# Kernel tuning notes

Measured on AMD Instinct MI355X. Metric: run time of the kernel, lower is better.

The kernel has to match this reference:

```python
import jax, jax.numpy as jnp
import numpy as np

DIM = 256
N_EMBED = 8192


def setup_inputs() -> dict:
    key = jax.random.key(0)
    k1, k2 = jax.random.split(key)
    x = jax.random.normal(k1, (16, 32, 32, DIM), dtype=jnp.float32)
    embed = jax.random.normal(k2, (DIM, N_EMBED), dtype=jnp.float32)
    return {"x": x, "embed": embed}


def reference(x, embed):
    # x: [B, H, W, D]; embed: [D, K]
    D = embed.shape[0]
    flat = x.reshape(-1, D)  # [N, D]
    dist = (
        jnp.sum(flat * flat, axis=1, keepdims=True)
        - 2.0 * (flat @ embed)
        + jnp.sum(embed * embed, axis=0, keepdims=True)
    )  # [N, K]
    embed_ind = jnp.argmin(dist, axis=1)  # argmax of -dist
    embed_ind = embed_ind.reshape(x.shape[:-1])  # [B, H, W]
    quantize = jnp.take(embed.T, embed_ind, axis=0)  # [B, H, W, D]
    diff = jnp.mean((jax.lax.stop_gradient(quantize) - x) ** 2)
    quantize = x + jax.lax.stop_gradient(quantize - x)  # straight-through
    return quantize, diff, embed_ind
```

## Files before the change

kernel.cpp:

```cpp
#include <hip/hip_runtime.h>

typedef unsigned long long u64;
typedef unsigned short ushort_t;
typedef float f32x4 __attribute__((ext_vector_type(4)));
typedef short bf16x8 __attribute__((ext_vector_type(8)));
typedef unsigned short ushort8 __attribute__((ext_vector_type(8)));

#define D_DIM   256
#define N_ROWS  16384
#define K_CODES 8192
#define OFF_DIFF 4194304
#define OFF_IND  4194305

#define XH_OFF    0ULL
#define XL_OFF    8388608ULL
#define EHT_OFF   16777216ULL
#define ELT_OFF   20971520ULL
#define ETF_OFF   25165824ULL
#define ENORM_OFF 33554432ULL
#define KEYS_OFF  33587200ULL
#define PV1_OFF   33718272ULL
#define PIDX_OFF  37912576ULL
#define PV2_OFF   42106880ULL
#define WLC_OFF   46301184ULL
#define WL_OFF    46301440ULL
#define PART_OFF  46366976ULL
#define WS_NEED   46375168ULL

#define MARGIN_TH 0.08f

#define GLD(gp, lp) __builtin_amdgcn_global_load_lds( \
    (const __attribute__((address_space(1))) unsigned int*)(const void*)(gp), \
    (__attribute__((address_space(3))) unsigned int*)(void*)(lp), 16, 0, 0)

__device__ __forceinline__ unsigned int fsort(float f) {
    unsigned int u = __float_as_uint(f);
    return (u & 0x80000000u) ? ~u : (u | 0x80000000u);
}
__device__ __forceinline__ ushort_t f2bf(float f) {
    unsigned int u = __float_as_uint(f);
    unsigned int r = (u + 0x7fffu + ((u >> 16) & 1u)) >> 16;
    return (ushort_t)r;
}
__device__ __forceinline__ float bf2f(ushort_t h) {
    return __uint_as_float(((unsigned int)h) << 16);
}

__global__ __launch_bounds__(256) void k_prep(const float* __restrict__ x,
                                              const float* __restrict__ e,
                                              ushort_t* __restrict__ xh,
                                              ushort_t* __restrict__ xl,
                                              ushort_t* __restrict__ ehT,
                                              ushort_t* __restrict__ elT,
                                              float* __restrict__ enorm,
                                              int* __restrict__ wlc,
                                              float* __restrict__ out_diff) {
    __shared__ float tile[64][257];
    const int bid = blockIdx.x;
    const int t = threadIdx.x;
    if (bid < 2048) {
        int base = (bid * 256 + t) * 8;
        float4 v0 = *reinterpret_cast<const float4*>(&x[base]);
        float4 v1 = *reinterpret_cast<const float4*>(&x[base + 4]);
        float f[8] = {v0.x, v0.y, v0.z, v0.w, v1.x, v1.y, v1.z, v1.w};
        ushort8 h, l;
        #pragma unroll
        for (int i = 0; i < 8; ++i) {
            ushort_t hb = f2bf(f[i]);
            h[i] = hb;
            l[i] = f2bf(f[i] - bf2f(hb));
        }
        *reinterpret_cast<ushort8*>(&xh[base]) = h;
        *reinterpret_cast<ushort8*>(&xl[base]) = l;
    } else if (bid < 2176) {
        const int c0 = (bid - 2048) * 64;
        for (int it = 0; it < 64; ++it) {
            int d = it * 4 + (t >> 6);
            tile[t & 63][d] = e[d * K_CODES + c0 + (t & 63)];
        }
        __syncthreads();
        #pragma unroll
        for (int it = 0; it < 8; ++it) {
            int cc = it * 8 + (t >> 5);
            int d0 = (t & 31) * 8;
            ushort8 h8, l8;
            #pragma unroll
            for (int j = 0; j < 8; ++j) {
                float v = tile[cc][d0 + j];
                ushort_t hb = f2bf(v);
                h8[j] = hb;
                l8[j] = f2bf(v - bf2f(hb));
            }
            size_t o = (size_t)(c0 + cc) * 256 + d0;
            *reinterpret_cast<ushort8*>(&ehT[o]) = h8;
            *reinterpret_cast<ushort8*>(&elT[o]) = l8;
        }
    } else {
        int k = (bid - 2176) * 256 + t;
        float s = 0.f;
        #pragma unroll 8
        for (int d = 0; d < D_DIM; ++d) {
            float v = e[d * K_CODES + k];
            s = fmaf(v, v, s);
        }
        enorm[k] = s;
        if (k == 0) { *wlc = 0; out_diff[0] = 0.0f; }
    }
}

__global__ __launch_bounds__(256, 3) void k_mfma(const ushort_t* __restrict__ xh,
                                                 const ushort_t* __restrict__ xl,
                                                 const ushort_t* __restrict__ ehT,
                                                 const ushort_t* __restrict__ elT,
                                                 const float* __restrict__ enorm,
                                                 float* __restrict__ pv1,
                                                 int* __restrict__ pidx,
                                                 float* __restrict__ pv2) {
    __shared__ short Ah[4096], Al[4096], Bh[4096], Bl[4096];
    __shared__ float mg_v1[2][128];
    __shared__ float mg_v2[2][128];
    __shared__ int   mg_i1[2][128];
    const int tid = threadIdx.x;
    const int l = tid & 63, w = tid >> 6;
    const int wm = w >> 1, wn = w & 1;
    const int r0 = blockIdx.x * 128;
    const int c0 = blockIdx.y * 128;

    const int rl = l >> 2;
    const int g = (l & 3) ^ ((rl >> 1) & 3);
    const int rowL0 = w * 32 + rl;
    const size_t aoff = (size_t)(c0 + rowL0) * 256 + g * 8;
    const size_t boff = (size_t)(r0 + rowL0) * 256 + g * 8;
    short* Adst  = Ah + w * 1024;
    short* Aldst = Al + w * 1024;
    short* Bdst  = Bh + w * 1024;
    short* Bldst = Bl + w * 1024;

    const int fr = l & 15, kg = l >> 4;

    f32x4 acc[4][4];
    #pragma unroll
    for (int mi = 0; mi < 4; ++mi)
        #pragma unroll
        for (int ni = 0; ni < 4; ++ni)
            #pragma unroll
            for (int q = 0; q < 4; ++q) acc[mi][ni][q] = 0.f;

    for (int kt = 0; kt < 8; ++kt) {
        const int ko = kt * 32;
        GLD(&ehT[aoff + ko], Adst);
        GLD(&ehT[aoff + ko + 4096], Adst + 512);
        GLD(&elT[aoff + ko], Aldst);
        GLD(&elT[aoff + ko + 4096], Aldst + 512);
        GLD(&xh[boff + ko], Bdst);
        GLD(&xh[boff + ko + 4096], Bdst + 512);
        GLD(&xl[boff + ko], Bldst);
        GLD(&xl[boff + ko + 4096], Bldst + 512);
        __syncthreads();

        bf16x8 a_h[4], a_l[4], b_h[4], b_l[4];
        #pragma unroll
        for (int mi = 0; mi < 4; ++mi) {
            int rf = wn * 64 + mi * 16 + fr;
            int idx = rf * 32 + ((kg ^ ((rf >> 1) & 3)) * 8);
            a_h[mi] = *reinterpret_cast<const bf16x8*>(&Ah[idx]);
            a_l[mi] = *reinterpret_cast<const bf16x8*>(&Al[idx]);
        }
        #pragma unroll
        for (int ni = 0; ni < 4; ++ni) {
            int cf = wm * 64 + ni * 16 + fr;
            int idx = cf * 32 + ((kg ^ ((cf >> 1) & 3)) * 8);
            b_h[ni] = *reinterpret_cast<const bf16x8*>(&Bh[idx]);
            b_l[ni] = *reinterpret_cast<const bf16x8*>(&Bl[idx]);
        }
        #pragma unroll
        for (int mi = 0; mi < 4; ++mi)
            #pragma unroll
            for (int ni = 0; ni < 4; ++ni) {
                acc[mi][ni] = __builtin_amdgcn_mfma_f32_16x16x32_bf16(a_h[mi], b_h[ni], acc[mi][ni], 0, 0, 0);
                acc[mi][ni] = __builtin_amdgcn_mfma_f32_16x16x32_bf16(a_h[mi], b_l[ni], acc[mi][ni], 0, 0, 0);
                acc[mi][ni] = __builtin_amdgcn_mfma_f32_16x16x32_bf16(a_l[mi], b_h[ni], acc[mi][ni], 0, 0, 0);
            }
        __syncthreads();
    }

    float v1[4], v2[4];
    int   i1[4];
    #pragma unroll
    for (int ni = 0; ni < 4; ++ni) { v1[ni] = 1e30f; v2[ni] = 1e30f; i1[ni] = 0; }

    float en_r[4][4];
    #pragma unroll
    for (int mi = 0; mi < 4; ++mi)
        #pragma unroll
        for (int r = 0; r < 4; ++r)
            en_r[mi][r] = enorm[c0 + wn * 64 + mi * 16 + kg * 4 + r];
    const int cwn = c0 + wn * 64 + kg * 4;

    #pragma unroll
    for (int ni = 0; ni < 4; ++ni)
        #pragma unroll
        for (int mi = 0; mi < 4; ++mi)
            #pragma unroll
            for (int r = 0; r < 4; ++r) {
                float dv = fmaf(-2.f, acc[mi][ni][r], en_r[mi][r]);
                int c = cwn + mi * 16 + r;
                if (dv < v1[ni]) { v2[ni] = v1[ni]; v1[ni] = dv; i1[ni] = c; }
                else v2[ni] = fminf(v2[ni], dv);
            }

    #pragma unroll
    for (int ni = 0; ni < 4; ++ni) {
        #pragma unroll
        for (int m = 16; m <= 32; m <<= 1) {
            float ov1 = __shfl_xor(v1[ni], m, 64);
            int   oi1 = __shfl_xor(i1[ni], m, 64);
            float ov2 = __shfl_xor(v2[ni], m, 64);
            bool better = (ov1 < v1[ni]) || (ov1 == v1[ni] && oi1 < i1[ni]);
            float nv2 = fminf(fminf(v2[ni], ov2), better ? v1[ni] : ov1);
            if (better) { v1[ni] = ov1; i1[ni] = oi1; }
            v2[ni] = nv2;
        }
        if (l < 16) {
            int lr = wm * 64 + ni * 16 + l;
            mg_v1[wn][lr] = v1[ni];
            mg_i1[wn][lr] = i1[ni];
            mg_v2[wn][lr] = v2[ni];
        }
    }

    __syncthreads();
    if (tid < 128) {
        float v1a = mg_v1[0][tid], v2a = mg_v2[0][tid];
        float v1b = mg_v1[1][tid], v2b = mg_v2[1][tid];
        int   i1a = mg_i1[0][tid], i1b = mg_i1[1][tid];
        bool better = (v1b < v1a) || (v1b == v1a && i1b < i1a);
        float fv1 = better ? v1b : v1a;
        int   fi1 = better ? i1b : i1a;
        float fv2 = fminf(fminf(v2a, v2b), better ? v1a : v1b);
        int pos = (r0 + tid) * 64 + blockIdx.y;
        pv1[pos] = fv1; pidx[pos] = fi1; pv2[pos] = fv2;
    }
}

__global__ __launch_bounds__(256) void k_reduce(const float* __restrict__ pv1,
                                                const int* __restrict__ pidx,
                                                const float* __restrict__ pv2,
                                                u64* __restrict__ keys,
                                                int* __restrict__ wlc,
                                                int* __restrict__ wl) {
    const int w = threadIdx.x >> 6, l = threadIdx.x & 63;
    const int row = blockIdx.x * 4 + w;
    float v1 = pv1[row * 64 + l];
    int   i1 = pidx[row * 64 + l];
    float v2 = pv2[row * 64 + l];
    #pragma unroll
    for (int m = 1; m <= 32; m <<= 1) {
        float ov1 = __shfl_xor(v1, m, 64);
        int   oi1 = __shfl_xor(i1, m, 64);
        float ov2 = __shfl_xor(v2, m, 64);
        bool better = (ov1 < v1) || (ov1 == v1 && oi1 < i1);
        float nv2 = fminf(fminf(v2, ov2), better ? v1 : ov1);
        if (better) { v1 = ov1; i1 = oi1; }
        v2 = nv2;
    }
    if (l == 0) {
        if (v2 - v1 < MARGIN_TH) {
            int p = atomicAdd(wlc, 1);
            wl[p] = row;
            keys[row] = ~0ULL;
        } else {
            keys[row] = (((u64)fsort(v1)) << 32) | (unsigned int)i1;
        }
    }
}

__global__ __launch_bounds__(128) void k_exact(const float* __restrict__ x,
                                               const float* __restrict__ e,
                                               const float* __restrict__ enorm,
                                               const int* __restrict__ wlc,
                                               const int* __restrict__ wl,
                                               u64* __restrict__ keys) {
    __shared__ float xs[8][256];
    __shared__ int rowids[8];
    __shared__ u64 red[8][2];
    const int t = threadIdx.x;
    const int cnt = *wlc;
    const int c = blockIdx.x * 128 + t;
    const float en = enorm[c];

    for (int j = blockIdx.y; j * 8 < cnt; j += 16) {
        int nr = cnt - j * 8; if (nr > 8) nr = 8;
        if (t < 8) rowids[t] = (t < nr) ? wl[j * 8 + t] : 0;
        __syncthreads();
        for (int rr = 0; rr < nr; ++rr) {
            int row = rowids[rr];
            xs[rr][t] = x[(size_t)row * 256 + t];
            xs[rr][t + 128] = x[(size_t)row * 256 + t + 128];
        }
        __syncthreads();
        float dot[8];
        #pragma unroll
        for (int rr = 0; rr < 8; ++rr) dot[rr] = 0.f;
        for (int d = 0; d < 256; ++d) {
            float ev = e[d * K_CODES + c];
            #pragma unroll
            for (int rr = 0; rr < 8; ++rr) dot[rr] = fmaf(ev, xs[rr][d], dot[rr]);
        }
        #pragma unroll
        for (int rr = 0; rr < 8; ++rr) {
            float dist = fmaf(-2.f, dot[rr], en);
            u64 kk = (((u64)fsort(dist)) << 32) | (unsigned int)c;
            #pragma unroll
            for (int m = 1; m <= 32; m <<= 1) {
                u64 ok = __shfl_xor(kk, m, 64);
                kk = ok < kk ? ok : kk;
            }
            if ((t & 63) == 0) red[rr][t >> 6] = kk;
        }
        __syncthreads();
        if (t < nr) {
            u64 fk = red[t][0] < red[t][1] ? red[t][0] : red[t][1];
            atomicMin(&keys[rowids[t]], fk);
        }
        __syncthreads();
    }
}

__global__ __launch_bounds__(256) void k_gather2(const float* __restrict__ x,
                                                 const ushort_t* __restrict__ ehT,
                                                 const ushort_t* __restrict__ elT,
                                                 const u64* __restrict__ keys,
                                                 float* __restrict__ out_q,
                                                 float* __restrict__ out_ind,
                                                 float* __restrict__ out_diff) {
    const int t = threadIdx.x, w = t >> 6, l = t & 63;
    const int row = blockIdx.x * 8 + w * 2 + (l >> 5);
    const int d0 = (l & 31) * 8;
    const int idx = (int)(keys[row] & 0xFFFFFFFFu);

    ushort8 h8 = *reinterpret_cast<const ushort8*>(&ehT[(size_t)idx * 256 + d0]);
    ushort8 l8 = *reinterpret_cast<const ushort8*>(&elT[(size_t)idx * 256 + d0]);
    float4 xv0 = *reinterpret_cast<const float4*>(&x[(size_t)row * 256 + d0]);
    float4 xv1 = *reinterpret_cast<const float4*>(&x[(size_t)row * 256 + d0 + 4]);
    float xv[8] = {xv0.x, xv0.y, xv0.z, xv0.w, xv1.x, xv1.y, xv1.z, xv1.w};

    float q[8];
    float s = 0.f;
    #pragma unroll
    for (int j = 0; j < 8; ++j) {
        q[j] = bf2f(h8[j]) + bf2f(l8[j]);
        float dq = q[j] - xv[j];
        s = fmaf(dq, dq, s);
    }
    float4 q0 = {q[0], q[1], q[2], q[3]};
    float4 q1 = {q[4], q[5], q[6], q[7]};
    *reinterpret_cast<float4*>(&out_q[(size_t)row * 256 + d0]) = q0;
    *reinterpret_cast<float4*>(&out_q[(size_t)row * 256 + d0 + 4]) = q1;
    if (d0 == 0) out_ind[row] = (float)idx;

    #pragma unroll
    for (int m = 1; m <= 32; m <<= 1) s += __shfl_xor(s, m, 64);
    __shared__ float red[4];
    if (l == 0) red[w] = s;
    __syncthreads();
    if (t == 0)
        atomicAdd(out_diff, (red[0] + red[1] + red[2] + red[3]) * (1.0f / 4194304.0f));
}

__global__ __launch_bounds__(256) void k_norms(const float* __restrict__ e,
                                               float* __restrict__ enorm,
                                               int* __restrict__ wlc) {
    int k = blockIdx.x * 256 + threadIdx.x;
    float s = 0.f;
    #pragma unroll 8
    for (int d = 0; d < D_DIM; ++d) {
        float v = e[d * K_CODES + k];
        s = fmaf(v, v, s);
    }
    enorm[k] = s;
    if (k == 0) *wlc = 0;
}

constexpr int FBM = 64, FBN = 256, FBK = 32, FNSPLIT = 2;

__global__ __launch_bounds__(256) void k_init_fb(u64* __restrict__ keys,
                                                 float* __restrict__ diff_slot) {
    int t = blockIdx.x * 256 + threadIdx.x;
    if (t < N_ROWS) keys[t] = ~0ULL;
    if (t == 0) diff_slot[0] = 0.0f;
}

__global__ __launch_bounds__(256) void k_argmin_fb(const float* __restrict__ x,
                                                   const float* __restrict__ e,
                                                   const float* __restrict__ enorm,
                                                   u64* __restrict__ keys) {
    __shared__ float xs[FBK][FBM + 4];
    __shared__ float es[FBK][FBN];
    const int tid = threadIdx.x;
    const int tr = tid >> 5, tc = tid & 31;
    const int row0 = blockIdx.x * FBM;
    const int cbase = blockIdx.y * (K_CODES / FNSPLIT);
    float minv[8]; int mini[8];
    #pragma unroll
    for (int i = 0; i < 8; ++i) { minv[i] = 1e30f; mini[i] = 0; }
    for (int chunk = 0; chunk < (K_CODES / FNSPLIT) / FBN; ++chunk) {
        const int c0 = cbase + chunk * FBN;
        float acc[8][8];
        #pragma unroll
        for (int i = 0; i < 8; ++i)
            #pragma unroll
            for (int j = 0; j < 8; ++j) acc[i][j] = 0.f;
        for (int kt = 0; kt < D_DIM / FBK; ++kt) {
            #pragma unroll
            for (int l2 = 0; l2 < 2; ++l2) {
                int q = tid + 256 * l2, r = q >> 3, kq = q & 7;
                float4 v = *reinterpret_cast<const float4*>(&x[(row0 + r) * D_DIM + kt * FBK + kq * 4]);
                xs[kq * 4 + 0][r] = v.x; xs[kq * 4 + 1][r] = v.y;
                xs[kq * 4 + 2][r] = v.z; xs[kq * 4 + 3][r] = v.w;
            }
            #pragma unroll
            for (int l2 = 0; l2 < 8; ++l2) {
                int q = tid + 256 * l2, k = q >> 6, cq = q & 63;
                float4 v = *reinterpret_cast<const float4*>(&e[(kt * FBK + k) * K_CODES + c0 + cq * 4]);
                *reinterpret_cast<float4*>(&es[k][cq * 4]) = v;
            }
            __syncthreads();
            #pragma unroll 8
            for (int k = 0; k < FBK; ++k) {
                float4 a0 = *reinterpret_cast<const float4*>(&xs[k][tr * 8]);
                float4 a1 = *reinterpret_cast<const float4*>(&xs[k][tr * 8 + 4]);
                float4 b0 = *reinterpret_cast<const float4*>(&es[k][tc * 8]);
                float4 b1 = *reinterpret_cast<const float4*>(&es[k][tc * 8 + 4]);
                float a[8] = {a0.x, a0.y, a0.z, a0.w, a1.x, a1.y, a1.z, a1.w};
                float b[8] = {b0.x, b0.y, b0.z, b0.w, b1.x, b1.y, b1.z, b1.w};
                #pragma unroll
                for (int i = 0; i < 8; ++i)
                    #pragma unroll
                    for (int j = 0; j < 8; ++j) acc[i][j] = fmaf(a[i], b[j], acc[i][j]);
            }
            __syncthreads();
        }
        #pragma unroll
        for (int j = 0; j < 8; ++j) {
            int c = c0 + tc * 8 + j;
            float en = enorm[c];
            #pragma unroll
            for (int i = 0; i < 8; ++i) {
                float dv = fmaf(-2.0f, acc[i][j], en);
                if (dv < minv[i]) { minv[i] = dv; mini[i] = c; }
            }
        }
    }
    #pragma unroll
    for (int m = 16; m >= 1; m >>= 1) {
        #pragma unroll
        for (int i = 0; i < 8; ++i) {
            float ov = __shfl_xor(minv[i], m, 64);
            int oi = __shfl_xor(mini[i], m, 64);
            if (ov < minv[i] || (ov == minv[i] && oi < mini[i])) { minv[i] = ov; mini[i] = oi; }
        }
    }
    if (tc == 0) {
        #pragma unroll
        for (int i = 0; i < 8; ++i) {
            int row = row0 + tr * 8 + i;
            u64 key = (((u64)fsort(minv[i])) << 32) | (unsigned int)mini[i];
            atomicMin(&keys[row], key);
        }
    }
}

__global__ __launch_bounds__(256) void k_gather_fb(const float* __restrict__ x,
                                                   const float* __restrict__ e,
                                                   const u64* __restrict__ keys,
                                                   float* __restrict__ out_q,
                                                   float* __restrict__ out_diff,
                                                   float* __restrict__ out_ind) {
    int row = blockIdx.x, d = threadIdx.x;
    int idx = (int)(keys[row] & 0xFFFFFFFFu);
    float q = e[d * K_CODES + idx];
    float xv = x[row * D_DIM + d];
    out_q[row * D_DIM + d] = q;
    if (d == 0) out_ind[row] = (float)idx;
    float sq = q - xv; sq *= sq;
    #pragma unroll
    for (int m = 32; m >= 1; m >>= 1) sq += __shfl_xor(sq, m, 64);
    __shared__ float red[4];
    if ((d & 63) == 0) red[d >> 6] = sq;
    __syncthreads();
    if (d == 0) {
        float s = (red[0] + red[1] + red[2] + red[3]) * (1.0f / (float)(N_ROWS * D_DIM));
        atomicAdd(out_diff, s);
    }
}

extern "C" void kernel_launch(void* const* d_in, const int* in_sizes, int n_in,
                              void* d_out, int out_size, void* d_ws, size_t ws_size,
                              hipStream_t stream) {
    const float* x = (const float*)d_in[0];
    const float* e = (const float*)d_in[1];
    float* out = (float*)d_out;
    float* out_q = out;
    float* out_diff = out + OFF_DIFF;
    float* out_ind = out + OFF_IND;
    char* ws = (char*)d_ws;

    if (ws_size >= WS_NEED) {
        ushort_t* xh  = (ushort_t*)(ws + XH_OFF);
        ushort_t* xl  = (ushort_t*)(ws + XL_OFF);
        ushort_t* ehT = (ushort_t*)(ws + EHT_OFF);
        ushort_t* elT = (ushort_t*)(ws + ELT_OFF);
        float* enorm  = (float*)(ws + ENORM_OFF);
        u64* keys     = (u64*)(ws + KEYS_OFF);
        float* pv1    = (float*)(ws + PV1_OFF);
        int* pidx     = (int*)(ws + PIDX_OFF);
        float* pv2    = (float*)(ws + PV2_OFF);
        int* wlc      = (int*)(ws + WLC_OFF);
        int* wl       = (int*)(ws + WL_OFF);

        k_prep   <<<2208, 256, 0, stream>>>(x, e, xh, xl, ehT, elT, enorm, wlc, out_diff);
        k_mfma   <<<dim3(128, 64), 256, 0, stream>>>(xh, xl, ehT, elT, enorm, pv1, pidx, pv2);
        k_reduce <<<4096, 256, 0, stream>>>(pv1, pidx, pv2, keys, wlc, wl);
        k_exact  <<<dim3(64, 16), 128, 0, stream>>>(x, e, enorm, wlc, wl, keys);
        k_gather2<<<2048, 256, 0, stream>>>(x, ehT, elT, keys, out_q, out_ind, out_diff);
    } else {
        float* enorm = (float*)ws;
        u64* keys = (u64*)(ws + 32768);
        k_init_fb  <<<64, 256, 0, stream>>>(keys, out_diff);
        k_norms    <<<32, 256, 0, stream>>>(e, enorm, (int*)(ws + 163840));
        k_argmin_fb<<<dim3(N_ROWS / FBM, FNSPLIT), 256, 0, stream>>>(x, e, enorm, keys);
        k_gather_fb<<<N_ROWS, 256, 0, stream>>>(x, e, keys, out_q, out_diff, out_ind);
    }
}
```

Before: 351.0 us.

## Fuse reduce, exact rescoring and gather into one kernel; shrink prep LDS tile

```diff
diff --git a/kernel.cpp b/kernel.cpp
--- a/kernel.cpp
+++ b/kernel.cpp
@@ -5,6 +5,7 @@
 typedef float f32x4 __attribute__((ext_vector_type(4)));
 typedef short bf16x8 __attribute__((ext_vector_type(8)));
 typedef unsigned short ushort8 __attribute__((ext_vector_type(8)));
+typedef unsigned short ushort4v __attribute__((ext_vector_type(4)));
 
 #define D_DIM   256
 #define N_ROWS  16384
@@ -16,15 +17,12 @@
 #define XL_OFF    8388608ULL
 #define EHT_OFF   16777216ULL
 #define ELT_OFF   20971520ULL
-#define ETF_OFF   25165824ULL
 #define ENORM_OFF 33554432ULL
 #define KEYS_OFF  33587200ULL
 #define PV1_OFF   33718272ULL
 #define PIDX_OFF  37912576ULL
 #define PV2_OFF   42106880ULL
 #define WLC_OFF   46301184ULL
-#define WL_OFF    46301440ULL
-#define PART_OFF  46366976ULL
 #define WS_NEED   46375168ULL
 
 #define MARGIN_TH 0.08f
@@ -53,9 +51,8 @@
                                               ushort_t* __restrict__ ehT,
                                               ushort_t* __restrict__ elT,
                                               float* __restrict__ enorm,
-                                              int* __restrict__ wlc,
                                               float* __restrict__ out_diff) {
-    __shared__ float tile[64][257];
+    __shared__ float tile[64][65];
     const int bid = blockIdx.x;
     const int t = threadIdx.x;
     if (bid < 2048) {
@@ -74,26 +71,31 @@
         *reinterpret_cast<ushort8*>(&xl[base]) = l;
     } else if (bid < 2176) {
         const int c0 = (bid - 2048) * 64;
-        for (int it = 0; it < 64; ++it) {
-            int d = it * 4 + (t >> 6);
-            tile[t & 63][d] = e[d * K_CODES + c0 + (t & 63)];
-        }
-        __syncthreads();
-        #pragma unroll
-        for (int it = 0; it < 8; ++it) {
-            int cc = it * 8 + (t >> 5);
-            int d0 = (t & 31) * 8;
-            ushort8 h8, l8;
-            #pragma unroll
-            for (int j = 0; j < 8; ++j) {
-                float v = tile[cc][d0 + j];
-                ushort_t hb = f2bf(v);
-                h8[j] = hb;
-                l8[j] = f2bf(v - bf2f(hb));
-            }
-            size_t o = (size_t)(c0 + cc) * 256 + d0;
-            *reinterpret_cast<ushort8*>(&ehT[o]) = h8;
-            *reinterpret_cast<ushort8*>(&elT[o]) = l8;
+        for (int dc = 0; dc < 4; ++dc) {
+            const int d0c = dc * 64;
+            if (dc) __syncthreads();
+            #pragma unroll
+            for (int it = 0; it < 16; ++it) {
+                int dl = it * 4 + (t >> 6);
+                tile[t & 63][dl] = e[(d0c + dl) * K_CODES + c0 + (t & 63)];
+            }
+            __syncthreads();
+            #pragma unroll
+            for (int rep = 0; rep < 2; ++rep) {
+                int q2 = t + rep * 256;
+                int cc = q2 >> 3, grp = q2 & 7;
+                ushort8 h8, l8;
+                #pragma unroll
+                for (int j = 0; j < 8; ++j) {
+                    float v = tile[cc][grp * 8 + j];
+                    ushort_t hb = f2bf(v);
+                    h8[j] = hb;
+                    l8[j] = f2bf(v - bf2f(hb));
+                }
+                size_t o = (size_t)(c0 + cc) * 256 + d0c + grp * 8;
+                *reinterpret_cast<ushort8*>(&ehT[o]) = h8;
+                *reinterpret_cast<ushort8*>(&elT[o]) = l8;
+            }
         }
     } else {
         int k = (bid - 2176) * 256 + t;
@@ -104,7 +106,7 @@
             s = fmaf(v, v, s);
         }
         enorm[k] = s;
-        if (k == 0) { *wlc = 0; out_diff[0] = 0.0f; }
+        if (k == 0) out_diff[0] = 0.0f;
     }
 }
 
@@ -243,14 +245,25 @@
     }
 }
 
-__global__ __launch_bounds__(256) void k_reduce(const float* __restrict__ pv1,
-                                                const int* __restrict__ pidx,
-                                                const float* __restrict__ pv2,
-                                                u64* __restrict__ keys,
-                                                int* __restrict__ wlc,
-                                                int* __restrict__ wl) {
-    const int w = threadIdx.x >> 6, l = threadIdx.x & 63;
+__global__ __launch_bounds__(256) void k_fin(const float* __restrict__ x,
+                                             const float* __restrict__ e,
+                                             const ushort_t* __restrict__ ehT,
+                                             const ushort_t* __restrict__ elT,
+                                             const float* __restrict__ enorm,
+                                             const float* __restrict__ pv1,
+                                             const int* __restrict__ pidx,
+                                             const float* __restrict__ pv2,
+                                             float* __restrict__ out_q,
+                                             float* __restrict__ out_ind,
+                                             float* __restrict__ out_diff) {
+    __shared__ u64   rowkey[4];
+    __shared__ int   rowflag[4];
+    __shared__ float xs[256];
+    __shared__ u64   bred[4];
+    __shared__ float dred[4];
+    const int t = threadIdx.x, w = t >> 6, l = t & 63;
     const int row = blockIdx.x * 4 + w;
+
     float v1 = pv1[row * 64 + l];
     int   i1 = pidx[row * 64 + l];
     float v2 = pv2[row * 64 + l];
@@ -265,107 +278,71 @@
         v2 = nv2;
     }
     if (l == 0) {
-        if (v2 - v1 < MARGIN_TH) {
-            int p = atomicAdd(wlc, 1);
-            wl[p] = row;
-            keys[row] = ~0ULL;
-        } else {
-            keys[row] = (((u64)fsort(v1)) << 32) | (unsigned int)i1;
-        }
-    }
-}
-
-__global__ __launch_bounds__(128) void k_exact(const float* __restrict__ x,
-                                               const float* __restrict__ e,
-                                               const float* __restrict__ enorm,
-                                               const int* __restrict__ wlc,
-                                               const int* __restrict__ wl,
-                                               u64* __restrict__ keys) {
-    __shared__ float xs[8][256];
-    __shared__ int rowids[8];
-    __shared__ u64 red[8][2];
-    const int t = threadIdx.x;
-    const int cnt = *wlc;
-    const int c = blockIdx.x * 128 + t;
-    const float en = enorm[c];
-
-    for (int j = blockIdx.y; j * 8 < cnt; j += 16) {
-        int nr = cnt - j * 8; if (nr > 8) nr = 8;
-        if (t < 8) rowids[t] = (t < nr) ? wl[j * 8 + t] : 0;
+        rowflag[w] = (v2 - v1 < MARGIN_TH) ? 1 : 0;
+        rowkey[w]  = (((u64)fsort(v1)) << 32) | (unsigned int)i1;
+    }
+    __syncthreads();
+
+    for (int w2 = 0; w2 < 4; ++w2) {
+        if (!rowflag[w2]) continue;
+        const int r2 = blockIdx.x * 4 + w2;
+        xs[t] = x[(size_t)r2 * 256 + t];
         __syncthreads();
-        for (int rr = 0; rr < nr; ++rr) {
-            int row = rowids[rr];
-            xs[rr][t] = x[(size_t)row * 256 + t];
-            xs[rr][t + 128] = x[(size_t)row * 256 + t + 128];
-        }
+        u64 best = ~0ULL;
+        for (int cb = 0; cb < 8; ++cb) {
+            int cA = cb * 1024 + t;
+            float dot[4] = {0.f, 0.f, 0.f, 0.f};
+            for (int d = 0; d < 256; ++d) {
+                float xv = xs[d];
+                const float* ed = &e[(size_t)d * K_CODES + cA];
+                dot[0] = fmaf(ed[0],   xv, dot[0]);
+                dot[1] = fmaf(ed[256], xv, dot[1]);
+                dot[2] = fmaf(ed[512], xv, dot[2]);
+                dot[3] = fmaf(ed[768], xv, dot[3]);
+            }
+            #pragma unroll
+            for (int q = 0; q < 4; ++q) {
+                int c = cA + q * 256;
+                float dist = fmaf(-2.f, dot[q], enorm[c]);
+                u64 kk = (((u64)fsort(dist)) << 32) | (unsigned int)c;
+                best = kk < best ? kk : best;
+            }
+        }
+        #pragma unroll
+        for (int m = 1; m <= 32; m <<= 1) {
+            u64 ok = __shfl_xor(best, m, 64);
+            best = ok < best ? ok : best;
+        }
+        if (l == 0) bred[w] = best;
         __syncthreads();
-        float dot[8];
-        #pragma unroll
-        for (int rr = 0; rr < 8; ++rr) dot[rr] = 0.f;
-        for (int d = 0; d < 256; ++d) {
-            float ev = e[d * K_CODES + c];
-            #pragma unroll
-            for (int rr = 0; rr < 8; ++rr) dot[rr] = fmaf(ev, xs[rr][d], dot[rr]);
-        }
-        #pragma unroll
-        for (int rr = 0; rr < 8; ++rr) {
-            float dist = fmaf(-2.f, dot[rr], en);
-            u64 kk = (((u64)fsort(dist)) << 32) | (unsigned int)c;
-            #pragma unroll
-            for (int m = 1; m <= 32; m <<= 1) {
-                u64 ok = __shfl_xor(kk, m, 64);
-                kk = ok < kk ? ok : kk;
-            }
-            if ((t & 63) == 0) red[rr][t >> 6] = kk;
+        if (t == 0) {
+            u64 b0 = bred[0] < bred[1] ? bred[0] : bred[1];
+            u64 b1 = bred[2] < bred[3] ? bred[2] : bred[3];
+            rowkey[w2] = b0 < b1 ? b0 : b1;
         }
         __syncthreads();
-        if (t < nr) {
-            u64 fk = red[t][0] < red[t][1] ? red[t][0] : red[t][1];
-            atomicMin(&keys[rowids[t]], fk);
-        }
-        __syncthreads();
-    }
-}
-
-__global__ __launch_bounds__(256) void k_gather2(const float* __restrict__ x,
-                                                 const ushort_t* __restrict__ ehT,
-                                                 const ushort_t* __restrict__ elT,
-                                                 const u64* __restrict__ keys,
-                                                 float* __restrict__ out_q,
-                                                 float* __restrict__ out_ind,
-                                                 float* __restrict__ out_diff) {
-    const int t = threadIdx.x, w = t >> 6, l = t & 63;
-    const int row = blockIdx.x * 8 + w * 2 + (l >> 5);
-    const int d0 = (l & 31) * 8;
-    const int idx = (int)(keys[row] & 0xFFFFFFFFu);
-
-    ushort8 h8 = *reinterpret_cast<const ushort8*>(&ehT[(size_t)idx * 256 + d0]);
-    ushort8 l8 = *reinterpret_cast<const ushort8*>(&elT[(size_t)idx * 256 + d0]);
-    float4 xv0 = *reinterpret_cast<const float4*>(&x[(size_t)row * 256 + d0]);
-    float4 xv1 = *reinterpret_cast<const float4*>(&x[(size_t)row * 256 + d0 + 4]);
-    float xv[8] = {xv0.x, xv0.y, xv0.z, xv0.w, xv1.x, xv1.y, xv1.z, xv1.w};
-
-    float q[8];
-    float s = 0.f;
-    #pragma unroll
-    for (int j = 0; j < 8; ++j) {
-        q[j] = bf2f(h8[j]) + bf2f(l8[j]);
-        float dq = q[j] - xv[j];
-        s = fmaf(dq, dq, s);
-    }
-    float4 q0 = {q[0], q[1], q[2], q[3]};
-    float4 q1 = {q[4], q[5], q[6], q[7]};
-    *reinterpret_cast<float4*>(&out_q[(size_t)row * 256 + d0]) = q0;
-    *reinterpret_cast<float4*>(&out_q[(size_t)row * 256 + d0 + 4]) = q1;
-    if (d0 == 0) out_ind[row] = (float)idx;
-
+    }
+
+    const int idx = (int)(rowkey[w] & 0xFFFFFFFFu);
+    ushort4v h4 = *reinterpret_cast<const ushort4v*>(&ehT[(size_t)idx * 256 + l * 4]);
+    ushort4v l4 = *reinterpret_cast<const ushort4v*>(&elT[(size_t)idx * 256 + l * 4]);
+    float4 xv = *reinterpret_cast<const float4*>(&x[(size_t)row * 256 + l * 4]);
+    float q0 = bf2f(h4[0]) + bf2f(l4[0]);
+    float q1 = bf2f(h4[1]) + bf2f(l4[1]);
+    float q2 = bf2f(h4[2]) + bf2f(l4[2]);
+    float q3 = bf2f(h4[3]) + bf2f(l4[3]);
+    float4 qv = {q0, q1, q2, q3};
+    *reinterpret_cast<float4*>(&out_q[(size_t)row * 256 + l * 4]) = qv;
+    if (l == 0) out_ind[row] = (float)idx;
+
+    float d0 = q0 - xv.x, d1 = q1 - xv.y, d2 = q2 - xv.z, d3 = q3 - xv.w;
+    float s = d0 * d0 + d1 * d1 + d2 * d2 + d3 * d3;
     #pragma unroll
     for (int m = 1; m <= 32; m <<= 1) s += __shfl_xor(s, m, 64);
-    __shared__ float red[4];
-    if (l == 0) red[w] = s;
+    if (l == 0) dred[w] = s;
     __syncthreads();
     if (t == 0)
-        atomicAdd(out_diff, (red[0] + red[1] + red[2] + red[3]) * (1.0f / 4194304.0f));
+        atomicAdd(out_diff, (dred[0] + dred[1] + dred[2] + dred[3]) * (1.0f / 4194304.0f));
 }
 
 __global__ __launch_bounds__(256) void k_norms(const float* __restrict__ e,
@@ -512,18 +489,14 @@
         ushort_t* ehT = (ushort_t*)(ws + EHT_OFF);
         ushort_t* elT = (ushort_t*)(ws + ELT_OFF);
         float* enorm  = (float*)(ws + ENORM_OFF);
-        u64* keys     = (u64*)(ws + KEYS_OFF);
         float* pv1    = (float*)(ws + PV1_OFF);
         int* pidx     = (int*)(ws + PIDX_OFF);
         float* pv2    = (float*)(ws + PV2_OFF);
-        int* wlc      = (int*)(ws + WLC_OFF);
-        int* wl       = (int*)(ws + WL_OFF);
-
-        k_prep   <<<2208, 256, 0, stream>>>(x, e, xh, xl, ehT, elT, enorm, wlc, out_diff);
-        k_mfma   <<<dim3(128, 64), 256, 0, stream>>>(xh, xl, ehT, elT, enorm, pv1, pidx, pv2);
-        k_reduce <<<4096, 256, 0, stream>>>(pv1, pidx, pv2, keys, wlc, wl);
-        k_exact  <<<dim3(64, 16), 128, 0, stream>>>(x, e, enorm, wlc, wl, keys);
-        k_gather2<<<2048, 256, 0, stream>>>(x, ehT, elT, keys, out_q, out_ind, out_diff);
+
+        k_prep<<<2208, 256, 0, stream>>>(x, e, xh, xl, ehT, elT, enorm, out_diff);
+        k_mfma<<<dim3(128, 64), 256, 0, stream>>>(xh, xl, ehT, elT, enorm, pv1, pidx, pv2);
+        k_fin <<<4096, 256, 0, stream>>>(x, e, ehT, elT, enorm, pv1, pidx, pv2,
+                                         out_q, out_ind, out_diff);
     } else {
         float* enorm = (float*)ws;
         u64* keys = (u64*)(ws + 32768);
```

Result: slower. 563.0 us (+60.4%).
